# Optimization experiments

Hardware: AMD Instinct MI355X
Metric: run time of the kernel (lower is better)

Reference implementation:

```python
import jax, jax.numpy as jnp
import numpy as np

N_EMBD = 768
N_HEAD = 12
HEAD_DIM = N_EMBD // N_HEAD
LN_EPS = 1e-5


def setup_inputs() -> dict:
    key = jax.random.key(0)
    ks = jax.random.split(key, 12)
    s = 0.02
    B, T = 8, 1024
    return {
        "x": jax.random.normal(ks[0], (B, T, N_EMBD), dtype=jnp.float32),
        "ln1_g": jnp.ones((N_EMBD,), jnp.float32),
        "ln1_b": jnp.zeros((N_EMBD,), jnp.float32),
        "w_attn": jax.random.normal(ks[1], (N_EMBD, 3 * N_EMBD), jnp.float32) * s,
        "b_attn": jnp.zeros((3 * N_EMBD,), jnp.float32),
        "w_proj": jax.random.normal(ks[2], (N_EMBD, N_EMBD), jnp.float32) * s,
        "b_proj": jnp.zeros((N_EMBD,), jnp.float32),
        "ln2_g": jnp.ones((N_EMBD,), jnp.float32),
        "ln2_b": jnp.zeros((N_EMBD,), jnp.float32),
        "w_fc1": jax.random.normal(ks[3], (N_EMBD, 4 * N_EMBD), jnp.float32) * s,
        "b_fc1": jnp.zeros((4 * N_EMBD,), jnp.float32),
        "w_fc2": jax.random.normal(ks[4], (4 * N_EMBD, N_EMBD), jnp.float32) * s,
        "b_fc2": jnp.zeros((N_EMBD,), jnp.float32),
    }


def _layernorm(x, g, b):
    mu = jnp.mean(x, axis=-1, keepdims=True)
    var = jnp.mean(jnp.square(x - mu), axis=-1, keepdims=True)
    return (x - mu) * jax.lax.rsqrt(var + LN_EPS) * g + b


def _block(x, ln1_g, ln1_b, w_attn, b_attn, w_proj, b_proj,
           ln2_g, ln2_b, w_fc1, b_fc1, w_fc2, b_fc2):
    B, T, C = x.shape
    # --- causal self-attention (dropout inactive in eval) ---
    h = _layernorm(x, ln1_g, ln1_b)
    qkv = h @ w_attn + b_attn                      # [B,T,3C]
    q, k, v = jnp.split(qkv, 3, axis=-1)
    q = q.reshape(B, T, N_HEAD, HEAD_DIM).transpose(0, 2, 1, 3)  # [B,H,T,D]
    k = k.reshape(B, T, N_HEAD, HEAD_DIM).transpose(0, 2, 1, 3)
    v = v.reshape(B, T, N_HEAD, HEAD_DIM).transpose(0, 2, 1, 3)
    att = jnp.einsum('bhtd,bhsd->bhts', q, k) * (1.0 / np.sqrt(HEAD_DIM))
    mask = jnp.tril(jnp.ones((T, T), dtype=bool))
    att = jnp.where(mask, att, -jnp.inf)
    att = jax.nn.softmax(att, axis=-1)
    y = jnp.einsum('bhts,bhsd->bhtd', att, v)
    y = y.transpose(0, 2, 1, 3).reshape(B, T, C)
    x = x + y @ w_proj + b_proj
    # --- MLP ---
    h2 = _layernorm(x, ln2_g, ln2_b)
    h2 = jax.nn.gelu(h2 @ w_fc1 + b_fc1, approximate=True)
    x = x + h2 @ w_fc2 + b_fc2
    return x


def reference(x, ln1_g, ln1_b, w_attn, b_attn, w_proj, b_proj,
              ln2_g, ln2_b, w_fc1, b_fc1, w_fc2, b_fc2):
    return _block(x, ln1_g, ln1_b, w_attn, b_attn, w_proj, b_proj,
                  ln2_g, ln2_b, w_fc1, b_fc1, w_fc2, b_fc2)
```

## Files before the change

### kernel.cpp

```cpp
#include <hip/hip_runtime.h>
#include <cstdint>
#include <cmath>

typedef unsigned short u16;
typedef __bf16 bf16_t;
typedef bf16_t bf16x8 __attribute__((ext_vector_type(8)));
typedef float f32x4 __attribute__((ext_vector_type(4)));
typedef u16 u16x8 __attribute__((ext_vector_type(8)));
typedef u16 u16x4 __attribute__((ext_vector_type(4)));

#define DEV __device__ __forceinline__

DEV u16 f2b(float f) {
    uint32_t u = __builtin_bit_cast(uint32_t, f);
    u += 0x7FFFu + ((u >> 16) & 1u);
    return (u16)(u >> 16);
}
DEV float b2f(u16 h) { return __builtin_bit_cast(float, (uint32_t)h << 16); }

DEV bf16x8 load8(const u16* p) {
    return __builtin_bit_cast(bf16x8, *reinterpret_cast<const u16x8*>(p));
}

DEV void async16(void* lds, const void* g) {
    __builtin_amdgcn_global_load_lds(
        reinterpret_cast<const __attribute__((address_space(1))) void*>(
            reinterpret_cast<uintptr_t>(g)),
        reinterpret_cast<__attribute__((address_space(3))) void*>(
            reinterpret_cast<uintptr_t>(lds)),
        16, 0, 0);
}

DEV float gelu_t(float x) {
    float z = 0.7978845608028654f * (x + 0.044715f * x * x * x);
    z = fminf(fmaxf(z, -15.0f), 15.0f);
    float e = __expf(2.0f * z);
    return 0.5f * x * (1.0f + (e - 1.0f) / (e + 1.0f));
}

__global__ __launch_bounds__(256) void ln_k(const float* __restrict__ x,
                                            const float* __restrict__ g,
                                            const float* __restrict__ bb,
                                            u16* __restrict__ out) {
    const int lane = threadIdx.x & 63, w = threadIdx.x >> 6;
    const int row = blockIdx.x * 4 + w;
    const float4* xr = reinterpret_cast<const float4*>(x + (size_t)row * 768);
    float4 v[3];
    float s = 0.f, s2 = 0.f;
#pragma unroll
    for (int i = 0; i < 3; ++i) {
        v[i] = xr[i * 64 + lane];
        s += v[i].x + v[i].y + v[i].z + v[i].w;
        s2 += v[i].x * v[i].x + v[i].y * v[i].y + v[i].z * v[i].z + v[i].w * v[i].w;
    }
#pragma unroll
    for (int off = 1; off < 64; off <<= 1) {
        s += __shfl_xor(s, off);
        s2 += __shfl_xor(s2, off);
    }
    const float mu = s * (1.0f / 768.0f);
    const float rstd = rsqrtf(s2 * (1.0f / 768.0f) - mu * mu + 1e-5f);
#pragma unroll
    for (int i = 0; i < 3; ++i) {
        int col = i * 256 + lane * 4;
        u16x4 o;
        o[0] = f2b((v[i].x - mu) * rstd * g[col + 0] + bb[col + 0]);
        o[1] = f2b((v[i].y - mu) * rstd * g[col + 1] + bb[col + 1]);
        o[2] = f2b((v[i].z - mu) * rstd * g[col + 2] + bb[col + 2]);
        o[3] = f2b((v[i].w - mu) * rstd * g[col + 3] + bb[col + 3]);
        *reinterpret_cast<u16x4*>(out + (size_t)row * 768 + col) = o;
    }
}

__global__ __launch_bounds__(256) void wconv_k(const float* __restrict__ W,
                                               u16* __restrict__ WT, int K, int N) {
    __shared__ float tile[32][33];
    const int tx = threadIdx.x, ty = threadIdx.y;
    const int n0 = blockIdx.x * 32, k0 = blockIdx.y * 32;
#pragma unroll
    for (int i = 0; i < 4; ++i)
        tile[ty + i * 8][tx] = W[(size_t)(k0 + ty + i * 8) * N + n0 + tx];
    __syncthreads();
#pragma unroll
    for (int i = 0; i < 4; ++i)
        WT[(size_t)(n0 + ty + i * 8) * K + k0 + tx] = f2b(tile[tx][ty + i * 8]);
}

__global__ __launch_bounds__(256) void vtrans_k(const u16* __restrict__ qkv,
                                                u16* __restrict__ vT) {
    __shared__ u16 tile[32][33];
    const int tx = threadIdx.x, ty = threadIdx.y;
    const int t0 = blockIdx.x * 32, d0 = blockIdx.y * 32, bh = blockIdx.z;
    const int b = bh / 12, hd = bh % 12;
#pragma unroll
    for (int i = 0; i < 4; ++i)
        tile[ty + i * 8][tx] =
            qkv[(size_t)(b * 1024 + t0 + ty + i * 8) * 2304 + 1536 + hd * 64 + d0 + tx];
    __syncthreads();
#pragma unroll
    for (int i = 0; i < 4; ++i)
        vT[(size_t)(bh * 64 + d0 + ty + i * 8) * 1024 + t0 + tx] = tile[tx][ty + i * 8];
}

template <int ACT, int RESID, int OUTBF>
__global__ __launch_bounds__(256) void gemm_bt(const u16* __restrict__ A,
                                               const u16* __restrict__ BT,
                                               const float* __restrict__ bias,
                                               const float* __restrict__ resid,
                                               void* __restrict__ out,
                                               int M, int N, int K) {
    __shared__ u16 As[3][128 * 32];
    __shared__ u16 Bs[3][128 * 32];
    const int tid = threadIdx.x, lane = tid & 63;
    const int l15 = lane & 15, lg = lane >> 4;
    const int nx = gridDim.x;
    const int bid = blockIdx.y * nx + blockIdx.x;
    const int q = (nx * gridDim.y) >> 3;
    const int swz = (bid & 7) * q + (bid >> 3);
    const int mBase = (swz / nx) * 128, nBase = (swz % nx) * 128;
    const int w = tid >> 6, wr = w >> 1, wc = w & 1;

    auto stage = [&](int buf, int kk) {
        const int k0 = kk << 5;
#pragma unroll
        for (int i = 0; i < 2; ++i) {
            int c = i * 256 + tid;
            int row = c >> 2, colE = (c & 3) << 3;
            async16(As[buf] + c * 8, A + (size_t)(mBase + row) * K + k0 + colE);
        }
#pragma unroll
        for (int i = 0; i < 2; ++i) {
            int c = i * 256 + tid;
            int row = c >> 2, colE = (c & 3) << 3;
            async16(Bs[buf] + c * 8, BT + (size_t)(nBase + row) * K + k0 + colE);
        }
    };

    f32x4 acc[4][4] = {};
    const int nsteps = K >> 5;
    stage(0, 0);
    stage(1, 1);
    int cur = 0;
    for (int kk = 0; kk < nsteps; ++kk) {
        if (kk + 2 < nsteps) {
            int nb = cur + 2;
            if (nb >= 3) nb -= 3;
            stage(nb, kk + 2);
            asm volatile("s_waitcnt vmcnt(8)" ::: "memory");
        } else if (kk + 1 < nsteps) {
            asm volatile("s_waitcnt vmcnt(4)" ::: "memory");
        } else {
            asm volatile("s_waitcnt vmcnt(0)" ::: "memory");
        }
        __builtin_amdgcn_s_barrier();
        asm volatile("" ::: "memory");

        bf16x8 af[4], bfr[4];
#pragma unroll
        for (int mi = 0; mi < 4; ++mi)
            af[mi] = load8(As[cur] + (wr * 64 + mi * 16 + l15) * 32 + lg * 8);
#pragma unroll
        for (int ni = 0; ni < 4; ++ni)
            bfr[ni] = load8(Bs[cur] + (wc * 64 + ni * 16 + l15) * 32 + lg * 8);
        __builtin_amdgcn_s_setprio(1);
#pragma unroll
        for (int mi = 0; mi < 4; ++mi)
#pragma unroll
            for (int ni = 0; ni < 4; ++ni)
                acc[mi][ni] = __builtin_amdgcn_mfma_f32_16x16x32_bf16(
                    af[mi], bfr[ni], acc[mi][ni], 0, 0, 0);
        __builtin_amdgcn_s_setprio(0);

        asm volatile("" ::: "memory");
        __builtin_amdgcn_s_barrier();
        cur = (cur == 2) ? 0 : cur + 1;
    }
#pragma unroll
    for (int mi = 0; mi < 4; ++mi) {
#pragma unroll
        for (int ni = 0; ni < 4; ++ni) {
            const int row0 = mBase + wr * 64 + mi * 16 + lg * 4;
            const int col = nBase + wc * 64 + ni * 16 + l15;
            const float bv = bias[col];
#pragma unroll
            for (int r = 0; r < 4; ++r) {
                float v = acc[mi][ni][r] + bv;
                if (ACT == 1) v = gelu_t(v);
                size_t off = (size_t)(row0 + r) * N + col;
                if (RESID) v += resid[off];
                if (OUTBF)
                    ((u16*)out)[off] = f2b(v);
                else
                    ((float*)out)[off] = v;
            }
        }
    }
}

__global__ __launch_bounds__(256, 3) void attn_k(const u16* __restrict__ qkv,
                                                 const u16* __restrict__ vT,
                                                 u16* __restrict__ y) {
    __shared__ u16 Ks[2][64 * 64];
    __shared__ u16 Vs[2][64 * 64];
    __shared__ u16 Ps[4][2][16 * 64];
    const int tid = threadIdx.x, lane = tid & 63, w = tid >> 6;
    const int bid = blockIdx.x;
    const uint32_t permPk = 2u | (7u << 3) | (1u << 6) | (4u << 9) | (6u << 12) |
                            (0u << 15) | (5u << 18) | (3u << 21);
    const int qt = (permPk >> (((bid + (bid >> 8)) & 7) * 3)) & 7;
    const int bh = ((bid >> 8) << 5) + ((bid & 255) >> 3);
    const int b = bh / 12, hd = bh % 12;
    const int l15 = lane & 15, lg = lane >> 4;
    const int r0 = qt * 128 + w * 32;

    const float qscale = 0.125f * 1.4426950408889634f;
    bf16x8 qf[2][2];
#pragma unroll
    for (int m = 0; m < 2; ++m) {
        const u16* qb = qkv + (size_t)(b * 1024 + r0 + m * 16 + l15) * 2304 + hd * 64;
#pragma unroll
        for (int ks = 0; ks < 2; ++ks) {
            u16x8 u = *reinterpret_cast<const u16x8*>(qb + ks * 32 + lg * 8);
            u16x8 o;
#pragma unroll
            for (int jj = 0; jj < 8; ++jj) o[jj] = f2b(b2f(u[jj]) * qscale);
            qf[m][ks] = __builtin_bit_cast(bf16x8, o);
        }
    }

    const u16* kbase = qkv + (size_t)(b * 1024) * 2304 + 768 + hd * 64;
    const u16* vbase = vT + (size_t)(bh * 64) * 1024;

    auto stage = [&](int buf, int j) {
#pragma unroll
        for (int i = 0; i < 2; ++i) {
            int c = i * 256 + tid;
            int row = c >> 3, sc = ((c & 7) ^ (row & 7)) << 3;
            async16(Ks[buf] + c * 8, kbase + (size_t)(j * 64 + row) * 2304 + sc);
        }
#pragma unroll
        for (int i = 0; i < 2; ++i) {
            int c = i * 256 + tid;
            int row = c >> 3, sc = ((c & 7) ^ (row & 7)) << 3;
            async16(Vs[buf] + c * 8, vbase + (size_t)row * 1024 + j * 64 + sc);
        }
    };

    f32x4 oacc[2][4] = {};
    float mrow[2] = {-1e30f, -1e30f};
    float lrow[2] = {0.f, 0.f};

    const int jd = (r0 + 31) >> 6;
    const int jmax = qt * 2 + 1;

    stage(0, 0);
    for (int j = 0; j <= jmax; ++j) {
        const int cur = j & 1;
        if (j < jmax) {
            stage(cur ^ 1, j + 1);
            asm volatile("s_waitcnt vmcnt(4)" ::: "memory");
        } else {
            asm volatile("s_waitcnt vmcnt(0)" ::: "memory");
        }
        __builtin_amdgcn_s_barrier();
        asm volatile("" ::: "memory");

        if (j <= jd) {
            const bool diag = (j == jd);
            const u16* Kc = Ks[cur];
            const u16* Vc = Vs[cur];
            f32x4 s[2][4] = {};
            __builtin_amdgcn_s_setprio(1);
#pragma unroll
            for (int ks = 0; ks < 2; ++ks) {
                bf16x8 kf[4];
#pragma unroll
                for (int ni = 0; ni < 4; ++ni) {
                    int key = ni * 16 + l15;
                    kf[ni] = load8(Kc + key * 64 + (((ks * 4 + lg) ^ (key & 7)) << 3));
                }
#pragma unroll
                for (int ni = 0; ni < 4; ++ni) {
                    s[0][ni] = __builtin_amdgcn_mfma_f32_16x16x32_bf16(
                        kf[ni], qf[0][ks], s[0][ni], 0, 0, 0);
                    s[1][ni] = __builtin_amdgcn_mfma_f32_16x16x32_bf16(
                        kf[ni], qf[1][ks], s[1][ni], 0, 0, 0);
                }
            }
            __builtin_amdgcn_s_setprio(0);

#pragma unroll
            for (int m = 0; m < 2; ++m) {
                if (diag) {
                    const int qrow = r0 + m * 16 + l15;
#pragma unroll
                    for (int ni = 0; ni < 4; ++ni) {
                        int key = j * 64 + ni * 16 + lg * 4;
#pragma unroll
                        for (int r = 0; r < 4; ++r)
                            if (key + r > qrow) s[m][ni][r] = -1e30f;
                    }
                }
                float pmax = -1e30f;
#pragma unroll
                for (int ni = 0; ni < 4; ++ni)
#pragma unroll
                    for (int r = 0; r < 4; ++r) pmax = fmaxf(pmax, s[m][ni][r]);
                pmax = fmaxf(pmax, __shfl_xor(pmax, 16));
                pmax = fmaxf(pmax, __shfl_xor(pmax, 32));

                if (!__all(pmax <= mrow[m] + 8.0f)) {
                    float mnew = fmaxf(mrow[m], pmax);
                    float scal = exp2f(mrow[m] - mnew);
                    mrow[m] = mnew;
                    lrow[m] *= scal;
#pragma unroll
                    for (int r = 0; r < 4; ++r) {
                        float sr = __shfl(scal, lg * 4 + r);
#pragma unroll
                        for (int ni = 0; ni < 4; ++ni) oacc[m][ni][r] *= sr;
                    }
                }
                float psum = 0.f;
#pragma unroll
                for (int ni = 0; ni < 4; ++ni) {
                    u16x4 pk;
#pragma unroll
                    for (int r = 0; r < 4; ++r) {
                        float pv = exp2f(s[m][ni][r] - mrow[m]);
                        psum += pv;
                        pk[r] = f2b(pv);
                    }
                    *reinterpret_cast<u16x4*>(
                        &Ps[w][m][l15 * 64 + ((ni * 16 + lg * 4) ^ ((l15 & 7) << 3))]) =
                        pk;
                }
                psum += __shfl_xor(psum, 16);
                psum += __shfl_xor(psum, 32);
                lrow[m] += psum;
            }

            __builtin_amdgcn_s_setprio(1);
#pragma unroll
            for (int ks = 0; ks < 2; ++ks) {
                bf16x8 pf0 = load8(
                    &Ps[w][0][l15 * 64 + ((ks * 32 + lg * 8) ^ ((l15 & 7) << 3))]);
                bf16x8 pf1 = load8(
                    &Ps[w][1][l15 * 64 + ((ks * 32 + lg * 8) ^ ((l15 & 7) << 3))]);
                bf16x8 vf[4];
#pragma unroll
                for (int ni = 0; ni < 4; ++ni) {
                    int d = ni * 16 + l15;
                    vf[ni] = load8(Vc + d * 64 + (((ks * 4 + lg) ^ (d & 7)) << 3));
                }
#pragma unroll
                for (int ni = 0; ni < 4; ++ni) {
                    oacc[0][ni] = __builtin_amdgcn_mfma_f32_16x16x32_bf16(
                        pf0, vf[ni], oacc[0][ni], 0, 0, 0);
                    oacc[1][ni] = __builtin_amdgcn_mfma_f32_16x16x32_bf16(
                        pf1, vf[ni], oacc[1][ni], 0, 0, 0);
                }
            }
            __builtin_amdgcn_s_setprio(0);
        }
        asm volatile("" ::: "memory");
        __builtin_amdgcn_s_barrier();
        asm volatile("" ::: "memory");
    }

#pragma unroll
    for (int m = 0; m < 2; ++m) {
#pragma unroll
        for (int r = 0; r < 4; ++r) {
            float rl = 1.0f / __shfl(lrow[m], lg * 4 + r);
            int row = r0 + m * 16 + lg * 4 + r;
#pragma unroll
            for (int ni = 0; ni < 4; ++ni) {
                int col = hd * 64 + ni * 16 + l15;
                y[(size_t)(b * 1024 + row) * 768 + col] = f2b(oacc[m][ni][r] * rl);
            }
        }
    }
}

extern "C" void kernel_launch(void* const* d_in, const int* in_sizes, int n_in,
                              void* d_out, int out_size, void* d_ws, size_t ws_size,
                              hipStream_t stream) {
    const float* x      = (const float*)d_in[0];
    const float* ln1_g  = (const float*)d_in[1];
    const float* ln1_b  = (const float*)d_in[2];
    const float* w_attn = (const float*)d_in[3];
    const float* b_attn = (const float*)d_in[4];
    const float* w_proj = (const float*)d_in[5];
    const float* b_proj = (const float*)d_in[6];
    const float* ln2_g  = (const float*)d_in[7];
    const float* ln2_b  = (const float*)d_in[8];
    const float* w_fc1  = (const float*)d_in[9];
    const float* b_fc1  = (const float*)d_in[10];
    const float* w_fc2  = (const float*)d_in[11];
    const float* b_fc2  = (const float*)d_in[12];
    float* out = (float*)d_out;

    char* p = (char*)d_ws;
    auto take = [&](size_t n) {
        char* r = p;
        p += (n + 255) & ~(size_t)255;
        return r;
    };
    u16* wT_attn = (u16*)take((size_t)2304 * 768 * 2);
    u16* wT_proj = (u16*)take((size_t)768 * 768 * 2);
    u16* wT_fc1  = (u16*)take((size_t)3072 * 768 * 2);
    u16* wT_fc2  = (u16*)take((size_t)768 * 3072 * 2);
    u16* h       = (u16*)take((size_t)8192 * 768 * 2);
    u16* bufA    = (u16*)take((size_t)50331648);
    u16* yb      = (u16*)take((size_t)8192 * 768 * 2);
    float* x1    = (float*)take((size_t)8192 * 768 * 4);
    u16* qkv = bufA;
    u16* vT  = bufA + (size_t)8192 * 2304;
    u16* g1  = bufA;

    const dim3 tb(32, 8);
    wconv_k<<<dim3(2304 / 32, 768 / 32), tb, 0, stream>>>(w_attn, wT_attn, 768, 2304);
    wconv_k<<<dim3(768 / 32, 768 / 32), tb, 0, stream>>>(w_proj, wT_proj, 768, 768);
    wconv_k<<<dim3(3072 / 32, 768 / 32), tb, 0, stream>>>(w_fc1, wT_fc1, 768, 3072);
    wconv_k<<<dim3(768 / 32, 3072 / 32), tb, 0, stream>>>(w_fc2, wT_fc2, 3072, 768);
    ln_k<<<2048, 256, 0, stream>>>(x, ln1_g, ln1_b, h);
    gemm_bt<0, 0, 1><<<dim3(18, 64), 256, 0, stream>>>(h, wT_attn, b_attn, nullptr,
                                                       qkv, 8192, 2304, 768);
    vtrans_k<<<dim3(32, 2, 96), tb, 0, stream>>>(qkv, vT);
    attn_k<<<768, 256, 0, stream>>>(qkv, vT, yb);
    gemm_bt<0, 1, 0><<<dim3(6, 64), 256, 0, stream>>>(yb, wT_proj, b_proj, x,
                                                      x1, 8192, 768, 768);
    ln_k<<<2048, 256, 0, stream>>>(x1, ln2_g, ln2_b, h);
    gemm_bt<1, 0, 1><<<dim3(24, 64), 256, 0, stream>>>(h, wT_fc1, b_fc1, nullptr,
                                                       g1, 8192, 3072, 768);
    gemm_bt<0, 1, 0><<<dim3(6, 64), 256, 0, stream>>>(g1, wT_fc2, b_fc2, x1,
                                                      out, 8192, 768, 3072);
}
```

Before: 260.4 us.

## Replace 128x128 GEMM with 256x256-tile, 512-thread, 4-slot swizzled pipeline

Swaps the 128x128, 256-thread, triple-buffered GEMM for a 256x256 tile computed by 8 waves. Each wave now owns 128x64 outputs. LDS becomes four slots with an XOR swizzle on the 16-byte column groups to reduce bank conflicts, and the K loop drops to one barrier per iteration. The next A and B tiles are staged in two halves interleaved with two MFMA phases, aiming for more data reuse per LDS byte and better overlap of loads with compute. In exchange, the N=768 GEMMs now launch only 96 blocks and QKV launches 288, which may leave many CUs idle. The roughly 128 KB of LDS also limits occupancy to one block per CU.

```diff
diff --git a/kernel.cpp b/kernel.cpp
--- a/kernel.cpp
+++ b/kernel.cpp
@@ -103,51 +103,54 @@
 }
 
 template <int ACT, int RESID, int OUTBF>
-__global__ __launch_bounds__(256) void gemm_bt(const u16* __restrict__ A,
-                                               const u16* __restrict__ BT,
-                                               const float* __restrict__ bias,
-                                               const float* __restrict__ resid,
-                                               void* __restrict__ out,
-                                               int M, int N, int K) {
-    __shared__ u16 As[3][128 * 32];
-    __shared__ u16 Bs[3][128 * 32];
+__global__ __launch_bounds__(512, 2) void gemm256(const u16* __restrict__ A,
+                                                  const u16* __restrict__ BT,
+                                                  const float* __restrict__ bias,
+                                                  const float* __restrict__ resid,
+                                                  void* __restrict__ out,
+                                                  int M, int N, int K) {
+    __shared__ u16 As[4][256 * 32];
+    __shared__ u16 Bs[4][256 * 32];
     const int tid = threadIdx.x, lane = tid & 63;
     const int l15 = lane & 15, lg = lane >> 4;
-    const int nx = gridDim.x;
-    const int bid = blockIdx.y * nx + blockIdx.x;
-    const int q = (nx * gridDim.y) >> 3;
+    const int w = tid >> 6, wr = w >> 2, wc = w & 3;
+    const int gx = gridDim.x;
+    const int bid = blockIdx.y * gx + blockIdx.x;
+    const int q = (gx * gridDim.y) >> 3;
     const int swz = (bid & 7) * q + (bid >> 3);
-    const int mBase = (swz / nx) * 128, nBase = (swz % nx) * 128;
-    const int w = tid >> 6, wr = w >> 1, wc = w & 1;
-
-    auto stage = [&](int buf, int kk) {
-        const int k0 = kk << 5;
+    const int mBase = (swz / gx) * 256, nBase = (swz % gx) * 256;
+
+    auto stageA = [&](int slot, int t) {
 #pragma unroll
         for (int i = 0; i < 2; ++i) {
-            int c = i * 256 + tid;
-            int row = c >> 2, colE = (c & 3) << 3;
-            async16(As[buf] + c * 8, A + (size_t)(mBase + row) * K + k0 + colE);
-        }
+            int c = i * 512 + tid;
+            int row = c >> 2;
+            int g = (c & 3) ^ ((row >> 1) & 3);
+            async16(As[slot] + c * 8, A + (size_t)(mBase + row) * K + t * 32 + g * 8);
+        }
+    };
+    auto stageB = [&](int slot, int t) {
 #pragma unroll
         for (int i = 0; i < 2; ++i) {
-            int c = i * 256 + tid;
-            int row = c >> 2, colE = (c & 3) << 3;
-            async16(Bs[buf] + c * 8, BT + (size_t)(nBase + row) * K + k0 + colE);
+            int c = i * 512 + tid;
+            int row = c >> 2;
+            int g = (c & 3) ^ ((row >> 1) & 3);
+            async16(Bs[slot] + c * 8, BT + (size_t)(nBase + row) * K + t * 32 + g * 8);
         }
     };
 
-    f32x4 acc[4][4] = {};
-    const int nsteps = K >> 5;
-    stage(0, 0);
-    stage(1, 1);
-    int cur = 0;
-    for (int kk = 0; kk < nsteps; ++kk) {
-        if (kk + 2 < nsteps) {
-            int nb = cur + 2;
-            if (nb >= 3) nb -= 3;
-            stage(nb, kk + 2);
-            asm volatile("s_waitcnt vmcnt(8)" ::: "memory");
-        } else if (kk + 1 < nsteps) {
+    f32x4 acc[8][4] = {};
+    const int swzr = (l15 >> 1) & 3;
+    const int nk = K >> 5;
+
+    stageA(0, 0);
+    stageB(0, 0);
+    stageA(1, 1);
+    stageB(1, 1);
+
+    for (int t = 0; t < nk; ++t) {
+        const int slot = t & 3;
+        if (t + 1 < nk) {
             asm volatile("s_waitcnt vmcnt(4)" ::: "memory");
         } else {
             asm volatile("s_waitcnt vmcnt(0)" ::: "memory");
@@ -155,31 +158,50 @@
         __builtin_amdgcn_s_barrier();
         asm volatile("" ::: "memory");
 
-        bf16x8 af[4], bfr[4];
+        const u16* Ab = As[slot];
+        const u16* Bb = Bs[slot];
+        if (t + 2 < nk) stageA((t + 2) & 3, t + 2);
+        bf16x8 bf[4], af[4];
+#pragma unroll
+        for (int ni = 0; ni < 4; ++ni)
+            bf[ni] = load8(Bb + (wc * 64 + ni * 16 + l15) * 32 + ((lg ^ swzr) << 3));
 #pragma unroll
         for (int mi = 0; mi < 4; ++mi)
-            af[mi] = load8(As[cur] + (wr * 64 + mi * 16 + l15) * 32 + lg * 8);
-#pragma unroll
-        for (int ni = 0; ni < 4; ++ni)
-            bfr[ni] = load8(Bs[cur] + (wc * 64 + ni * 16 + l15) * 32 + lg * 8);
+            af[mi] = load8(Ab + (wr * 128 + mi * 16 + l15) * 32 + ((lg ^ swzr) << 3));
+        asm volatile("s_waitcnt lgkmcnt(0)" ::: "memory");
+        __builtin_amdgcn_sched_barrier(0);
         __builtin_amdgcn_s_setprio(1);
 #pragma unroll
         for (int mi = 0; mi < 4; ++mi)
 #pragma unroll
             for (int ni = 0; ni < 4; ++ni)
                 acc[mi][ni] = __builtin_amdgcn_mfma_f32_16x16x32_bf16(
-                    af[mi], bfr[ni], acc[mi][ni], 0, 0, 0);
+                    af[mi], bf[ni], acc[mi][ni], 0, 0, 0);
         __builtin_amdgcn_s_setprio(0);
-
+        if (t + 2 < nk) stageB((t + 2) & 3, t + 2);
+        bf16x8 af2[4];
+#pragma unroll
+        for (int mi = 0; mi < 4; ++mi)
+            af2[mi] =
+                load8(Ab + (wr * 128 + 64 + mi * 16 + l15) * 32 + ((lg ^ swzr) << 3));
+        asm volatile("s_waitcnt lgkmcnt(0)" ::: "memory");
+        __builtin_amdgcn_sched_barrier(0);
+        __builtin_amdgcn_s_setprio(1);
+#pragma unroll
+        for (int mi = 0; mi < 4; ++mi)
+#pragma unroll
+            for (int ni = 0; ni < 4; ++ni)
+                acc[mi + 4][ni] = __builtin_amdgcn_mfma_f32_16x16x32_bf16(
+                    af2[mi], bf[ni], acc[mi + 4][ni], 0, 0, 0);
+        __builtin_amdgcn_s_setprio(0);
         asm volatile("" ::: "memory");
-        __builtin_amdgcn_s_barrier();
-        cur = (cur == 2) ? 0 : cur + 1;
-    }
-#pragma unroll
-    for (int mi = 0; mi < 4; ++mi) {
+    }
+
+#pragma unroll
+    for (int mi = 0; mi < 8; ++mi) {
 #pragma unroll
         for (int ni = 0; ni < 4; ++ni) {
-            const int row0 = mBase + wr * 64 + mi * 16 + lg * 4;
+            const int row0 = mBase + wr * 128 + mi * 16 + lg * 4;
             const int col = nBase + wc * 64 + ni * 16 + l15;
             const float bv = bias[col];
 #pragma unroll
@@ -425,15 +447,15 @@
     wconv_k<<<dim3(3072 / 32, 768 / 32), tb, 0, stream>>>(w_fc1, wT_fc1, 768, 3072);
     wconv_k<<<dim3(768 / 32, 3072 / 32), tb, 0, stream>>>(w_fc2, wT_fc2, 3072, 768);
     ln_k<<<2048, 256, 0, stream>>>(x, ln1_g, ln1_b, h);
-    gemm_bt<0, 0, 1><<<dim3(18, 64), 256, 0, stream>>>(h, wT_attn, b_attn, nullptr,
-                                                       qkv, 8192, 2304, 768);
+    gemm256<0, 0, 1><<<dim3(9, 32), 512, 0, stream>>>(h, wT_attn, b_attn, nullptr,
+                                                      qkv, 8192, 2304, 768);
     vtrans_k<<<dim3(32, 2, 96), tb, 0, stream>>>(qkv, vT);
     attn_k<<<768, 256, 0, stream>>>(qkv, vT, yb);
-    gemm_bt<0, 1, 0><<<dim3(6, 64), 256, 0, stream>>>(yb, wT_proj, b_proj, x,
+    gemm256<0, 1, 0><<<dim3(3, 32), 512, 0, stream>>>(yb, wT_proj, b_proj, x,
                                                       x1, 8192, 768, 768);
     ln_k<<<2048, 256, 0, stream>>>(x1, ln2_g, ln2_b, h);
-    gemm_bt<1, 0, 1><<<dim3(24, 64), 256, 0, stream>>>(h, wT_fc1, b_fc1, nullptr,
+    gemm256<1, 0, 1><<<dim3(12, 32), 512, 0, stream>>>(h, wT_fc1, b_fc1, nullptr,
                                                        g1, 8192, 3072, 768);
-    gemm_bt<0, 1, 0><<<dim3(6, 64), 256, 0, stream>>>(g1, wT_fc2, b_fc2, x1,
+    gemm256<0, 1, 0><<<dim3(3, 32), 512, 0, stream>>>(g1, wT_fc2, b_fc2, x1,
                                                       out, 8192, 768, 3072);
 }
```

Result: slower. 310.8 us (+19.4%).

## Use 256x256 GEMM tiles for QKV and FC1, store residual in bf16

Applied to the files above, without the earlier changes.

Adds a 512-thread GEMM kernel with 256x256 output tiles and double-buffered LDS, used for the wide QKV and FC1 GEMMs. Larger tiles cut global and LDS traffic per FLOP but raise register pressure and shrink the grid. The intermediate residual x1 is now stored as bf16 instead of fp32, with a bf16-input layernorm and bf16 residual reads, which halves that tensor's traffic at some cost in precision.

```diff
diff --git a/kernel.cpp b/kernel.cpp
--- a/kernel.cpp
+++ b/kernel.cpp
@@ -72,6 +72,44 @@
     }
 }
 
+__global__ __launch_bounds__(256) void ln_b16(const u16* __restrict__ x,
+                                              const float* __restrict__ g,
+                                              const float* __restrict__ bb,
+                                              u16* __restrict__ out) {
+    const int lane = threadIdx.x & 63, w = threadIdx.x >> 6;
+    const int row = blockIdx.x * 4 + w;
+    const u16* xr = x + (size_t)row * 768;
+    float v[12];
+    float s = 0.f, s2 = 0.f;
+#pragma unroll
+    for (int i = 0; i < 3; ++i) {
+        u16x4 u = *reinterpret_cast<const u16x4*>(xr + i * 256 + lane * 4);
+#pragma unroll
+        for (int jj = 0; jj < 4; ++jj) {
+            float f = b2f(u[jj]);
+            v[i * 4 + jj] = f;
+            s += f;
+            s2 += f * f;
+        }
+    }
+#pragma unroll
+    for (int off = 1; off < 64; off <<= 1) {
+        s += __shfl_xor(s, off);
+        s2 += __shfl_xor(s2, off);
+    }
+    const float mu = s * (1.0f / 768.0f);
+    const float rstd = rsqrtf(s2 * (1.0f / 768.0f) - mu * mu + 1e-5f);
+#pragma unroll
+    for (int i = 0; i < 3; ++i) {
+        int col = i * 256 + lane * 4;
+        u16x4 o;
+#pragma unroll
+        for (int jj = 0; jj < 4; ++jj)
+            o[jj] = f2b((v[i * 4 + jj] - mu) * rstd * g[col + jj] + bb[col + jj]);
+        *reinterpret_cast<u16x4*>(out + (size_t)row * 768 + col) = o;
+    }
+}
+
 __global__ __launch_bounds__(256) void wconv_k(const float* __restrict__ W,
                                                u16* __restrict__ WT, int K, int N) {
     __shared__ float tile[32][33];
@@ -102,11 +140,11 @@
         vT[(size_t)(bh * 64 + d0 + ty + i * 8) * 1024 + t0 + tx] = tile[tx][ty + i * 8];
 }
 
-template <int ACT, int RESID, int OUTBF>
+template <int ACT, int RESIDT, int OUTBF>
 __global__ __launch_bounds__(256) void gemm_bt(const u16* __restrict__ A,
                                                const u16* __restrict__ BT,
                                                const float* __restrict__ bias,
-                                               const float* __restrict__ resid,
+                                               const void* __restrict__ resid,
                                                void* __restrict__ out,
                                                int M, int N, int K) {
     __shared__ u16 As[3][128 * 32];
@@ -187,7 +225,122 @@
                 float v = acc[mi][ni][r] + bv;
                 if (ACT == 1) v = gelu_t(v);
                 size_t off = (size_t)(row0 + r) * N + col;
-                if (RESID) v += resid[off];
+                if (RESIDT == 1) v += ((const float*)resid)[off];
+                if (RESIDT == 2) v += b2f(((const u16*)resid)[off]);
+                if (OUTBF)
+                    ((u16*)out)[off] = f2b(v);
+                else
+                    ((float*)out)[off] = v;
+            }
+        }
+    }
+}
+
+template <int ACT, int RESIDT, int OUTBF>
+__global__ __launch_bounds__(512, 2) void gemm256(const u16* __restrict__ A,
+                                                  const u16* __restrict__ BT,
+                                                  const float* __restrict__ bias,
+                                                  const void* __restrict__ resid,
+                                                  void* __restrict__ out,
+                                                  int M, int N, int K) {
+    __shared__ u16 As[2][256 * 32];
+    __shared__ u16 Bs[2][256 * 32];
+    const int tid = threadIdx.x, lane = tid & 63;
+    const int l15 = lane & 15, lg = lane >> 4;
+    const int w = tid >> 6, wr = w >> 2, wc = w & 3;
+    const int gx = gridDim.x;
+    const int bid = blockIdx.y * gx + blockIdx.x;
+    const int q = (gx * gridDim.y) >> 3;
+    const int swz = (bid & 7) * q + (bid >> 3);
+    const int mBase = (swz / gx) * 256, nBase = (swz % gx) * 256;
+
+    auto stage = [&](int slot, int t) {
+#pragma unroll
+        for (int i = 0; i < 2; ++i) {
+            int c = i * 512 + tid;
+            int row = c >> 2;
+            int g = (c & 3) ^ ((row >> 1) & 3);
+            async16(As[slot] + c * 8, A + (size_t)(mBase + row) * K + t * 32 + g * 8);
+        }
+#pragma unroll
+        for (int i = 0; i < 2; ++i) {
+            int c = i * 512 + tid;
+            int row = c >> 2;
+            int g = (c & 3) ^ ((row >> 1) & 3);
+            async16(Bs[slot] + c * 8, BT + (size_t)(nBase + row) * K + t * 32 + g * 8);
+        }
+    };
+
+    f32x4 acc[8][4] = {};
+    const int swzr = (l15 >> 1) & 3;
+    const int nk = K >> 5;
+
+    stage(0, 0);
+    for (int t = 0; t < nk; ++t) {
+        const int cur = t & 1;
+        if (t + 1 < nk) {
+            stage(cur ^ 1, t + 1);
+            asm volatile("s_waitcnt vmcnt(4)" ::: "memory");
+        } else {
+            asm volatile("s_waitcnt vmcnt(0)" ::: "memory");
+        }
+        __builtin_amdgcn_s_barrier();
+        asm volatile("" ::: "memory");
+
+        const u16* Ab = As[cur];
+        const u16* Bb = Bs[cur];
+        bf16x8 bf[4], af[4];
+#pragma unroll
+        for (int ni = 0; ni < 4; ++ni)
+            bf[ni] = load8(Bb + (wc * 64 + ni * 16 + l15) * 32 + ((lg ^ swzr) << 3));
+#pragma unroll
+        for (int mi = 0; mi < 4; ++mi)
+            af[mi] = load8(Ab + (wr * 128 + mi * 16 + l15) * 32 + ((lg ^ swzr) << 3));
+        asm volatile("s_waitcnt lgkmcnt(0)" ::: "memory");
+        __builtin_amdgcn_sched_barrier(0);
+        __builtin_amdgcn_s_setprio(1);
+#pragma unroll
+        for (int mi = 0; mi < 4; ++mi)
+#pragma unroll
+            for (int ni = 0; ni < 4; ++ni)
+                acc[mi][ni] = __builtin_amdgcn_mfma_f32_16x16x32_bf16(
+                    af[mi], bf[ni], acc[mi][ni], 0, 0, 0);
+        __builtin_amdgcn_s_setprio(0);
+        bf16x8 af2[4];
+#pragma unroll
+        for (int mi = 0; mi < 4; ++mi)
+            af2[mi] =
+                load8(Ab + (wr * 128 + 64 + mi * 16 + l15) * 32 + ((lg ^ swzr) << 3));
+        asm volatile("s_waitcnt lgkmcnt(0)" ::: "memory");
+        __builtin_amdgcn_sched_barrier(0);
+        __builtin_amdgcn_s_setprio(1);
+#pragma unroll
+        for (int mi = 0; mi < 4; ++mi)
+#pragma unroll
+            for (int ni = 0; ni < 4; ++ni)
+                acc[mi + 4][ni] = __builtin_amdgcn_mfma_f32_16x16x32_bf16(
+                    af2[mi], bf[ni], acc[mi + 4][ni], 0, 0, 0);
+        __builtin_amdgcn_s_setprio(0);
+
+        asm volatile("" ::: "memory");
+        __builtin_amdgcn_s_barrier();
+        asm volatile("" ::: "memory");
+    }
+
+#pragma unroll
+    for (int mi = 0; mi < 8; ++mi) {
+#pragma unroll
+        for (int ni = 0; ni < 4; ++ni) {
+            const int row0 = mBase + wr * 128 + mi * 16 + lg * 4;
+            const int col = nBase + wc * 64 + ni * 16 + l15;
+            const float bv = bias[col];
+#pragma unroll
+            for (int r = 0; r < 4; ++r) {
+                float v = acc[mi][ni][r] + bv;
+                if (ACT == 1) v = gelu_t(v);
+                size_t off = (size_t)(row0 + r) * N + col;
+                if (RESIDT == 1) v += ((const float*)resid)[off];
+                if (RESIDT == 2) v += b2f(((const u16*)resid)[off]);
                 if (OUTBF)
                     ((u16*)out)[off] = f2b(v);
                 else
@@ -414,7 +567,7 @@
     u16* h       = (u16*)take((size_t)8192 * 768 * 2);
     u16* bufA    = (u16*)take((size_t)50331648);
     u16* yb      = (u16*)take((size_t)8192 * 768 * 2);
-    float* x1    = (float*)take((size_t)8192 * 768 * 4);
+    u16* x1b     = (u16*)take((size_t)8192 * 768 * 2);
     u16* qkv = bufA;
     u16* vT  = bufA + (size_t)8192 * 2304;
     u16* g1  = bufA;
@@ -425,15 +578,15 @@
     wconv_k<<<dim3(3072 / 32, 768 / 32), tb, 0, stream>>>(w_fc1, wT_fc1, 768, 3072);
     wconv_k<<<dim3(768 / 32, 3072 / 32), tb, 0, stream>>>(w_fc2, wT_fc2, 3072, 768);
     ln_k<<<2048, 256, 0, stream>>>(x, ln1_g, ln1_b, h);
-    gemm_bt<0, 0, 1><<<dim3(18, 64), 256, 0, stream>>>(h, wT_attn, b_attn, nullptr,
-                                                       qkv, 8192, 2304, 768);
+    gemm256<0, 0, 1><<<dim3(9, 32), 512, 0, stream>>>(h, wT_attn, b_attn, nullptr,
+                                                      qkv, 8192, 2304, 768);
     vtrans_k<<<dim3(32, 2, 96), tb, 0, stream>>>(qkv, vT);
     attn_k<<<768, 256, 0, stream>>>(qkv, vT, yb);
-    gemm_bt<0, 1, 0><<<dim3(6, 64), 256, 0, stream>>>(yb, wT_proj, b_proj, x,
-                                                      x1, 8192, 768, 768);
-    ln_k<<<2048, 256, 0, stream>>>(x1, ln2_g, ln2_b, h);
-    gemm_bt<1, 0, 1><<<dim3(24, 64), 256, 0, stream>>>(h, wT_fc1, b_fc1, nullptr,
+    gemm_bt<0, 1, 1><<<dim3(6, 64), 256, 0, stream>>>(yb, wT_proj, b_proj, x,
+                                                      x1b, 8192, 768, 768);
+    ln_b16<<<2048, 256, 0, stream>>>(x1b, ln2_g, ln2_b, h);
+    gemm256<1, 0, 1><<<dim3(12, 32), 512, 0, stream>>>(h, wT_fc1, b_fc1, nullptr,
                                                        g1, 8192, 3072, 768);
-    gemm_bt<0, 1, 0><<<dim3(6, 64), 256, 0, stream>>>(g1, wT_fc2, b_fc2, x1,
+    gemm_bt<0, 2, 0><<<dim3(6, 64), 256, 0, stream>>>(g1, wT_fc2, b_fc2, x1b,
                                                       out, 8192, 768, 3072);
 }
```

New measurement: 277.5 us. 1.07x slower.
